# Kernel tuning notes

Measured on AMD Instinct MI355X. Metric: run time of the kernel, lower is better.

Reference implementation:

```python
import jax, jax.numpy as jnp
import numpy as np

N = 100_000      # nodes
E = 1_600_000    # directed input edges (no self loops, unique canonical pairs)
F_IN = 256       # num_features
HID = 128        # 2 * num_hidden (GATConv out width)
NHID = 64        # num_hidden
C = 4            # num_classes
G = 128          # number of graphs in the batch
NEG_SLOPE = 0.2  # PyG GATConv default LeakyReLU slope


def setup_inputs() -> dict:
    key = jax.random.key(0)
    ks = jax.random.split(key, 16)

    # --- graph structure (numpy; deduped canonical pairs so that
    # concat(e, reversed(e)) exactly matches PyG to_undirected+coalesce) ---
    rng = np.random.RandomState(0)
    n_cand = int(E * 1.05)
    s = rng.randint(0, N, size=n_cand)
    off = rng.randint(1, N, size=n_cand)
    d = (s + off) % N                      # guarantees no self loops
    lo, hi = np.minimum(s, d), np.maximum(s, d)
    pairs = np.unique(lo.astype(np.int64) * N + hi.astype(np.int64))[:E]
    src = (pairs // N).astype(np.int64)
    dst = (pairs % N).astype(np.int64)
    edge_index = jnp.asarray(np.stack([src, dst]))  # [2, E]

    batch = jnp.sort(jax.random.randint(ks[0], (N,), 0, G)).astype(jnp.int64)
    x = jax.random.normal(ks[1], (N, F_IN), dtype=jnp.float32)

    sc = 0.05
    params = dict(
        W1=jax.random.normal(ks[2], (HID, F_IN)) * sc,
        as1=jax.random.normal(ks[3], (HID,)) * sc,
        ad1=jax.random.normal(ks[4], (HID,)) * sc,
        b1=jnp.zeros((HID,), jnp.float32),
        W2=jax.random.normal(ks[5], (HID, HID)) * sc,
        as2=jax.random.normal(ks[6], (HID,)) * sc,
        ad2=jax.random.normal(ks[7], (HID,)) * sc,
        b2=jnp.zeros((HID,), jnp.float32),
        fw1=jax.random.normal(ks[8], (NHID, HID)) * sc,
        fb1=jnp.zeros((NHID,), jnp.float32),
        fw2=jax.random.normal(ks[9], (C, NHID)) * sc,
        fb2=jnp.zeros((C,), jnp.float32),
    )
    return dict(x=x, edge_index=edge_index, batch=batch, **params)


def _gat_conv(h_in, src, dst, W, a_src, a_dst, bias):
    """PyG GATConv, heads=1, concat=True. src/dst include self loops."""
    h = h_in @ W.T                                        # [N, out]
    # per-edge attention logits: a_src . h_j + a_dst . h_i
    e = jax.nn.leaky_relu((h @ a_src)[src] + (h @ a_dst)[dst], NEG_SLOPE)
    # edge softmax over incoming edges of each dst node
    m = jax.ops.segment_max(e, dst, num_segments=N)       # [N]
    w = jnp.exp(e - m[dst])
    denom = jax.ops.segment_sum(w, dst, num_segments=N)   # [N] (>0: self loops)
    alpha = w / denom[dst]                                # [Etot]
    out = jax.ops.segment_sum(h[src] * alpha[:, None], dst, num_segments=N)
    return out + bias


def reference(x, edge_index, batch,
              W1, as1, ad1, b1, W2, as2, ad2, b2,
              fw1, fb1, fw2, fb2):
    # to_undirected: input has unique canonical (lo<hi) pairs -> concat exact
    s0, d0 = edge_index[0], edge_index[1]
    loop = jnp.arange(N, dtype=s0.dtype)
    src = jnp.concatenate([s0, d0, loop])  # GATConv adds self loops
    dst = jnp.concatenate([d0, s0, loop])

    h = jax.nn.selu(_gat_conv(x, src, dst, W1, as1, ad1, b1))
    h = jax.nn.selu(_gat_conv(h, src, dst, W2, as2, ad2, b2))

    # global mean pool over graphs
    sums = jax.ops.segment_sum(h, batch, num_segments=G)            # [G, HID]
    cnt = jax.ops.segment_sum(jnp.ones((N,), h.dtype), batch, num_segments=G)
    g = jax.nn.selu(sums / jnp.maximum(cnt, 1.0)[:, None])

    g = jax.nn.selu(g @ fw1.T + fb1)
    # dropout p=0.5 is identity in eval mode
    logits = g @ fw2.T + fb2
    return jax.nn.log_softmax(logits, axis=-1)                      # [G, C]
```

## Files before the change

### kernel.cpp

```cpp
#include <hip/hip_runtime.h>
#include <hip/hip_bf16.h>


#define NN 100000
#define EE 1600000
#define GG 128
#define HID 128
#define AGG_CAP 512
#define NEG_SLOPE 0.2f

__device__ __forceinline__ float lrelu(float x) { return x > 0.f ? x : NEG_SLOPE * x; }

__device__ __forceinline__ float selu(float x) {
    const float sc = 1.0507009873554805f, al = 1.6732632423543772f;
    return x > 0.f ? sc * x : sc * al * (__expf(x) - 1.f);
}

__device__ __forceinline__ unsigned short f2bf(float x) {
    unsigned int b = __float_as_uint(x);
    b += 0x7FFFu + ((b >> 16) & 1u);
    return (unsigned short)(b >> 16);
}


__global__ __launch_bounds__(256) void loptr_kernel(const int* __restrict__ ei,
                                                    int* __restrict__ loptr, int n, int E_) {
    int v = blockIdx.x * blockDim.x + threadIdx.x;
    if (v > n) return;
    int lo = 0, hi = E_;
    while (lo < hi) {
        int mid = (lo + hi) >> 1;
        if (ei[mid] < v) lo = mid + 1; else hi = mid;
    }
    loptr[v] = lo;
}


__global__ void count_kernel(const int* __restrict__ ei, int* __restrict__ deg, int E_) {
    int e = blockIdx.x * blockDim.x + threadIdx.x;
    if (e >= E_) return;
    atomicAdd(&deg[ei[E_ + e]], 1);
}

#define SCAN_CHUNK 512

__global__ __launch_bounds__(256) void block_sum_kernel(const int* __restrict__ deg,
                                                        int* __restrict__ bsum, int n) {
    __shared__ int sd[256];
    int b = blockIdx.x, t = threadIdx.x;
    int base = b * SCAN_CHUNK;
    int v = 0;
    int i0 = base + t, i1 = base + t + 256;
    if (i0 < n) v += deg[i0];
    if (i1 < n) v += deg[i1];
    sd[t] = v;
    __syncthreads();
    for (int off = 128; off; off >>= 1) {
        if (t < off) sd[t] += sd[t + off];
        __syncthreads();
    }
    if (t == 0) bsum[b] = sd[0];
}

__global__ __launch_bounds__(256) void top_scan_kernel(const int* __restrict__ bsum,
                                                       int* __restrict__ boff, int nb,
                                                       int* __restrict__ total_out) {
    __shared__ int a[256], b[256];
    int t = threadIdx.x;
    int v = (t < nb) ? bsum[t] : 0;
    int* cur = a; int* nxt = b;
    cur[t] = v;
    __syncthreads();
    for (int off = 1; off < 256; off <<= 1) {
        int val = cur[t] + ((t >= off) ? cur[t - off] : 0);
        nxt[t] = val;
        __syncthreads();
        int* tmp = cur; cur = nxt; nxt = tmp;
    }
    if (t < nb) boff[t] = cur[t] - v;
    if (t == nb - 1) *total_out = cur[t];
}

__global__ __launch_bounds__(512) void scan_final_kernel(const int* __restrict__ deg,
                                                         const int* __restrict__ boff,
                                                         int* __restrict__ row_ptr,
                                                         int* __restrict__ cursor, int n) {
    __shared__ int a[512], b[512];
    int blk = blockIdx.x, t = threadIdx.x;
    int i = blk * 512 + t;
    int v = (i < n) ? deg[i] : 0;
    int orig = v;
    int* cur = a; int* nxt = b;
    cur[t] = v;
    __syncthreads();
    for (int off = 1; off < 512; off <<= 1) {
        int val = cur[t] + ((t >= off) ? cur[t - off] : 0);
        nxt[t] = val;
        __syncthreads();
        int* tmp = cur; cur = nxt; nxt = tmp;
    }
    if (i < n) {
        int excl = cur[t] - orig + boff[blk];
        row_ptr[i] = excl;
        cursor[i] = excl;
    }
}

__global__ void scatter_kernel(const int* __restrict__ ei, int* __restrict__ cursor,
                               int* __restrict__ csr, int E_) {
    int e = blockIdx.x * blockDim.x + threadIdx.x;
    if (e >= E_) return;
    int u = ei[e], v = ei[E_ + e];
    int p = atomicAdd(&cursor[v], 1);
    csr[p] = u;
}


__global__ __launch_bounds__(256) void sgemm_nt(const float* __restrict__ A,
                                                const float* __restrict__ W,
                                                float* __restrict__ C,
                                                unsigned short* __restrict__ Cb,
                                                int M, int K) {
    __shared__ float As[32][128];
    __shared__ float Bs[32][128];
    int tid = threadIdx.x;
    int brow = blockIdx.x * 128;
    int tx = tid & 15, ty = tid >> 4;
    int lrow = tid >> 3;
    int lk4 = (tid & 7) << 2;
    float acc[8][8];
    #pragma unroll
    for (int i = 0; i < 8; ++i)
        #pragma unroll
        for (int j = 0; j < 8; ++j) acc[i][j] = 0.f;

    int kTiles = K >> 5;
    for (int kt = 0; kt < kTiles; ++kt) {
        int k0 = kt << 5;
        #pragma unroll
        for (int r = 0; r < 4; ++r) {
            int row = lrow + r * 32;
            int grow = brow + row;
            float4 v = make_float4(0.f, 0.f, 0.f, 0.f);
            if (grow < M) v = *reinterpret_cast<const float4*>(A + (size_t)grow * K + k0 + lk4);
            As[lk4 + 0][row] = v.x; As[lk4 + 1][row] = v.y;
            As[lk4 + 2][row] = v.z; As[lk4 + 3][row] = v.w;
        }
        #pragma unroll
        for (int r = 0; r < 4; ++r) {
            int col = lrow + r * 32;
            float4 v = *reinterpret_cast<const float4*>(W + (size_t)col * K + k0 + lk4);
            Bs[lk4 + 0][col] = v.x; Bs[lk4 + 1][col] = v.y;
            Bs[lk4 + 2][col] = v.z; Bs[lk4 + 3][col] = v.w;
        }
        __syncthreads();
        #pragma unroll
        for (int kk = 0; kk < 32; ++kk) {
            float ra[8], rb[8];
            #pragma unroll
            for (int i = 0; i < 8; ++i) ra[i] = As[kk][ty * 8 + i];
            #pragma unroll
            for (int j = 0; j < 8; ++j) rb[j] = Bs[kk][tx * 8 + j];
            #pragma unroll
            for (int i = 0; i < 8; ++i)
                #pragma unroll
                for (int j = 0; j < 8; ++j)
                    acc[i][j] = fmaf(ra[i], rb[j], acc[i][j]);
        }
        __syncthreads();
    }
    #pragma unroll
    for (int i = 0; i < 8; ++i) {
        int grow = brow + ty * 8 + i;
        if (grow < M) {
            float4* o = reinterpret_cast<float4*>(C + (size_t)grow * 128 + tx * 8);
            o[0] = make_float4(acc[i][0], acc[i][1], acc[i][2], acc[i][3]);
            o[1] = make_float4(acc[i][4], acc[i][5], acc[i][6], acc[i][7]);
            union { unsigned short u[8]; float4 f; } pk;
            #pragma unroll
            for (int j = 0; j < 8; ++j) pk.u[j] = f2bf(acc[i][j]);
            *reinterpret_cast<float4*>(Cb + (size_t)grow * 128 + tx * 8) = pk.f;
        }
    }
}


__global__ __launch_bounds__(256) void hshd_kernel(const float* __restrict__ h,
                                                   const float* __restrict__ a_src,
                                                   const float* __restrict__ a_dst,
                                                   float* __restrict__ hs, float* __restrict__ hd,
                                                   int n) {
    int w = (blockIdx.x * blockDim.x + threadIdx.x) >> 6;
    int lane = threadIdx.x & 63;
    if (w >= n) return;
    float2 hv = reinterpret_cast<const float2*>(h + (size_t)w * 128)[lane];
    float2 as2 = reinterpret_cast<const float2*>(a_src)[lane];
    float2 ad2 = reinterpret_cast<const float2*>(a_dst)[lane];
    float ps = hv.x * as2.x + hv.y * as2.y;
    float pd = hv.x * ad2.x + hv.y * ad2.y;
    #pragma unroll
    for (int off = 32; off; off >>= 1) {
        ps += __shfl_xor(ps, off);
        pd += __shfl_xor(pd, off);
    }
    if (lane == 0) { hs[w] = ps; hd[w] = pd; }
}


__global__ __launch_bounds__(256) void agg_kernel(const float* __restrict__ h,
                                                  const unsigned int* __restrict__ hb32,
                                                  const float* __restrict__ hs,
                                                  const float* __restrict__ hd,
                                                  const int* __restrict__ loptr,
                                                  const int* __restrict__ eiD,
                                                  const int* __restrict__ hiptr,
                                                  const int* __restrict__ csr,
                                                  const float* __restrict__ bias,
                                                  float* __restrict__ out, int n) {
    __shared__ float esh[4][AGG_CAP];
    __shared__ int ush[4][AGG_CAP];
    int wib = threadIdx.x >> 6;
    int lane = threadIdx.x & 63;
    int v = blockIdx.x * 4 + wib;
    if (v >= n) return;
    int s_lo = loptr[v];
    int dlo = loptr[v + 1] - s_lo;
    int s_hi = hiptr[v];
    int d = dlo + (hiptr[v + 1] - s_hi);
    float hdv = hd[v];
    float e_self = lrelu(hs[v] + hdv);
    float m, inv;
    bool fits = (d <= AGG_CAP);

    auto nbr = [&](int k) -> int {
        return (k < dlo) ? eiD[s_lo + k] : csr[s_hi + k - dlo];
    };
    auto gx = [&](int u) -> float2 {
        unsigned int w = hb32[(size_t)u * 64 + lane];
        return make_float2(__uint_as_float(w << 16), __uint_as_float(w & 0xFFFF0000u));
    };

    if (fits) {
        float mloc = -3.4e38f;
        for (int k = lane; k < d; k += 64) {
            int u = nbr(k);
            float e = lrelu(hs[u] + hdv);
            ush[wib][k] = u;
            esh[wib][k] = e;
            mloc = fmaxf(mloc, e);
        }
        #pragma unroll
        for (int off = 32; off; off >>= 1) mloc = fmaxf(mloc, __shfl_xor(mloc, off));
        m = fmaxf(mloc, e_self);
        float sloc = 0.f;
        for (int k = lane; k < d; k += 64) sloc += __expf(esh[wib][k] - m);
        #pragma unroll
        for (int off = 32; off; off >>= 1) sloc += __shfl_xor(sloc, off);
        float s = sloc + __expf(e_self - m);
        inv = 1.f / s;
        for (int k = lane; k < d; k += 64) esh[wib][k] = __expf(esh[wib][k] - m) * inv;
    } else {
        float mloc = -3.4e38f;
        for (int k = lane; k < d; k += 64) mloc = fmaxf(mloc, lrelu(hs[nbr(k)] + hdv));
        #pragma unroll
        for (int off = 32; off; off >>= 1) mloc = fmaxf(mloc, __shfl_xor(mloc, off));
        m = fmaxf(mloc, e_self);
        float sloc = 0.f;
        for (int k = lane; k < d; k += 64) sloc += __expf(lrelu(hs[nbr(k)] + hdv) - m);
        #pragma unroll
        for (int off = 32; off; off >>= 1) sloc += __shfl_xor(sloc, off);
        float s = sloc + __expf(e_self - m);
        inv = 1.f / s;
    }
    __syncthreads();

    float2 hvv = reinterpret_cast<const float2*>(h + (size_t)v * 128)[lane];
    float a_self = __expf(e_self - m) * inv;
    float accx = a_self * hvv.x;
    float accy = a_self * hvv.y;
    if (fits) {
        int k = 0;
        for (; k + 4 <= d; k += 4) {
            float a0 = esh[wib][k + 0], a1 = esh[wib][k + 1];
            float a2 = esh[wib][k + 2], a3 = esh[wib][k + 3];
            int u0 = ush[wib][k + 0], u1 = ush[wib][k + 1];
            int u2 = ush[wib][k + 2], u3 = ush[wib][k + 3];
            float2 x0 = gx(u0);
            float2 x1 = gx(u1);
            float2 x2 = gx(u2);
            float2 x3 = gx(u3);
            accx = fmaf(a0, x0.x, accx); accy = fmaf(a0, x0.y, accy);
            accx = fmaf(a1, x1.x, accx); accy = fmaf(a1, x1.y, accy);
            accx = fmaf(a2, x2.x, accx); accy = fmaf(a2, x2.y, accy);
            accx = fmaf(a3, x3.x, accx); accy = fmaf(a3, x3.y, accy);
        }
        for (; k < d; ++k) {
            float al = esh[wib][k];
            float2 xv = gx(ush[wib][k]);
            accx = fmaf(al, xv.x, accx);
            accy = fmaf(al, xv.y, accy);
        }
    } else {
        for (int k = 0; k < d; ++k) {
            int u = nbr(k);
            float al = __expf(lrelu(hs[u] + hdv) - m) * inv;
            float2 xv = gx(u);
            accx = fmaf(al, xv.x, accx);
            accy = fmaf(al, xv.y, accy);
        }
    }
    float2 bb = reinterpret_cast<const float2*>(bias)[lane];
    float o0 = selu(accx + bb.x);
    float o1 = selu(accy + bb.y);
    reinterpret_cast<float2*>(out + (size_t)v * 128)[lane] = make_float2(o0, o1);
}


__device__ __forceinline__ int lower_bound_dev(const int* __restrict__ b, int n, int val) {
    int lo = 0, hi = n;
    while (lo < hi) {
        int mid = (lo + hi) >> 1;
        if (b[mid] < val) lo = mid + 1; else hi = mid;
    }
    return lo;
}

__global__ __launch_bounds__(1024) void pool_mlp_kernel(const float* __restrict__ h,
                                                        const int* __restrict__ batch,
                                                        const float* __restrict__ fw1,
                                                        const float* __restrict__ fb1,
                                                        const float* __restrict__ fw2,
                                                        const float* __restrict__ fb2,
                                                        float* __restrict__ out, int n) {
    int g = blockIdx.x;
    int t = threadIdx.x;
    int lane = t & 63;
    int rg = t >> 6;
    __shared__ float2 sm[16][64];
    __shared__ float gv[128];
    __shared__ float hid[64];
    __shared__ float logits[4];

    int s = lower_bound_dev(batch, n, g);
    int e = lower_bound_dev(batch, n, g + 1);

    float2 acc = make_float2(0.f, 0.f);
    const float2* h2 = reinterpret_cast<const float2*>(h);
    int i = s + rg;
    for (; i + 16 < e; i += 32) {
        float2 v0 = h2[(size_t)i * 64 + lane];
        float2 v1 = h2[(size_t)(i + 16) * 64 + lane];
        acc.x += v0.x + v1.x;
        acc.y += v0.y + v1.y;
    }
    for (; i < e; i += 16) {
        float2 v0 = h2[(size_t)i * 64 + lane];
        acc.x += v0.x;
        acc.y += v0.y;
    }
    sm[rg][lane] = acc;
    __syncthreads();
    if (rg == 0) {
        float2 tot = make_float2(0.f, 0.f);
        #pragma unroll
        for (int r = 0; r < 16; ++r) {
            tot.x += sm[r][lane].x;
            tot.y += sm[r][lane].y;
        }
        float cnt = fmaxf((float)(e - s), 1.0f);
        gv[lane * 2 + 0] = selu(tot.x / cnt);
        gv[lane * 2 + 1] = selu(tot.y / cnt);
    }
    __syncthreads();
    if (t < 64) {
        float a = fb1[t];
        for (int k = 0; k < 128; ++k) a = fmaf(fw1[t * 128 + k], gv[k], a);
        hid[t] = selu(a);
    }
    __syncthreads();
    if (t < 4) {
        float a = fb2[t];
        for (int k = 0; k < 64; ++k) a = fmaf(fw2[t * 64 + k], hid[k], a);
        logits[t] = a;
    }
    __syncthreads();
    if (t < 4) {
        float mx = fmaxf(fmaxf(logits[0], logits[1]), fmaxf(logits[2], logits[3]));
        float sum = __expf(logits[0] - mx) + __expf(logits[1] - mx) +
                    __expf(logits[2] - mx) + __expf(logits[3] - mx);
        out[g * 4 + t] = logits[t] - mx - logf(sum);
    }
}


extern "C" void kernel_launch(void* const* d_in, const int* in_sizes, int n_in,
                              void* d_out, int out_size, void* d_ws, size_t ws_size,
                              hipStream_t stream) {
    const float* x   = (const float*)d_in[0];
    const int*   ei  = (const int*)d_in[1];
    const int*   bat = (const int*)d_in[2];
    const float* W1  = (const float*)d_in[3];
    const float* as1 = (const float*)d_in[4];
    const float* ad1 = (const float*)d_in[5];
    const float* b1  = (const float*)d_in[6];
    const float* W2  = (const float*)d_in[7];
    const float* as2 = (const float*)d_in[8];
    const float* ad2 = (const float*)d_in[9];
    const float* b2  = (const float*)d_in[10];
    const float* fw1 = (const float*)d_in[11];
    const float* fb1 = (const float*)d_in[12];
    const float* fw2 = (const float*)d_in[13];
    const float* fb2 = (const float*)d_in[14];
    float* out = (float*)d_out;

    char* ws = (char*)d_ws;
    size_t off = 0;
    auto alloc = [&](size_t bytes) {
        void* p = ws + off;
        off += (bytes + 255) & ~(size_t)255;
        return p;
    };
    float*          bufA    = (float*)alloc((size_t)NN * 128 * 4);
    float*          bufB    = (float*)alloc((size_t)NN * 128 * 4);
    unsigned short* hb      = (unsigned short*)alloc((size_t)NN * 128 * 2);
    float*          hs      = (float*)alloc((size_t)NN * 4);
    float*          hd      = (float*)alloc((size_t)NN * 4);
    int*            deg     = (int*)alloc((size_t)NN * 4);
    int*            row_ptr = (int*)alloc((size_t)(NN + 1) * 4);
    int*            cursor  = (int*)alloc((size_t)NN * 4);
    int*            loptr   = (int*)alloc((size_t)(NN + 1) * 4);
    int*            csr     = (int*)alloc((size_t)EE * 4);
    int*            bsum    = (int*)alloc(256 * 4);
    int*            boff    = (int*)alloc(256 * 4);

    hipMemsetAsync(deg, 0, (size_t)NN * 4, stream);
    loptr_kernel<<<(NN + 1 + 255) / 256, 256, 0, stream>>>(ei, loptr, NN, EE);
    count_kernel<<<(EE + 255) / 256, 256, 0, stream>>>(ei, deg, EE);
    int NB = (NN + SCAN_CHUNK - 1) / SCAN_CHUNK;
    block_sum_kernel<<<NB, 256, 0, stream>>>(deg, bsum, NN);
    top_scan_kernel<<<1, 256, 0, stream>>>(bsum, boff, NB, row_ptr + NN);
    scan_final_kernel<<<NB, 512, 0, stream>>>(deg, boff, row_ptr, cursor, NN);
    scatter_kernel<<<(EE + 255) / 256, 256, 0, stream>>>(ei, cursor, csr, EE);

    const int* eiD = ei + EE;

    sgemm_nt<<<(NN + 127) / 128, 256, 0, stream>>>(x, W1, bufA, hb, NN, 256);
    hshd_kernel<<<((size_t)NN * 64 + 255) / 256, 256, 0, stream>>>(bufA, as1, ad1, hs, hd, NN);
    agg_kernel<<<(NN + 3) / 4, 256, 0, stream>>>(bufA, (const unsigned int*)hb, hs, hd,
                                                 loptr, eiD, row_ptr, csr, b1, bufB, NN);

    sgemm_nt<<<(NN + 127) / 128, 256, 0, stream>>>(bufB, W2, bufA, hb, NN, 128);
    hshd_kernel<<<((size_t)NN * 64 + 255) / 256, 256, 0, stream>>>(bufA, as2, ad2, hs, hd, NN);
    agg_kernel<<<(NN + 3) / 4, 256, 0, stream>>>(bufA, (const unsigned int*)hb, hs, hd,
                                                 loptr, eiD, row_ptr, csr, b2, bufB, NN);

    pool_mlp_kernel<<<GG, 1024, 0, stream>>>(bufB, bat, fw1, fb1, fw2, fb2, out, NN);
}
```

Baseline: 828.8 us.

## Replace FP32 SIMT GEMMs with bf16 MFMA GEMMs and bf16 layer-2 input

```diff
diff --git a/kernel.cpp b/kernel.cpp
--- a/kernel.cpp
+++ b/kernel.cpp
@@ -9,6 +9,9 @@
 #define AGG_CAP 512
 #define NEG_SLOPE 0.2f
 
+typedef short bf16x8 __attribute__((ext_vector_type(8)));
+typedef float f32x4 __attribute__((ext_vector_type(4)));
+
 __device__ __forceinline__ float lrelu(float x) { return x > 0.f ? x : NEG_SLOPE * x; }
 
 __device__ __forceinline__ float selu(float x) {
@@ -20,6 +23,17 @@
     unsigned int b = __float_as_uint(x);
     b += 0x7FFFu + ((b >> 16) & 1u);
     return (unsigned short)(b >> 16);
+}
+
+
+__global__ __launch_bounds__(256) void castbf_kernel(const float* __restrict__ in,
+                                                     unsigned short* __restrict__ out, int n) {
+    int i = (blockIdx.x * blockDim.x + threadIdx.x) * 4;
+    if (i >= n) return;
+    float4 v = *reinterpret_cast<const float4*>(in + i);
+    union { unsigned short u[4]; uint2 w; } pk;
+    pk.u[0] = f2bf(v.x); pk.u[1] = f2bf(v.y); pk.u[2] = f2bf(v.z); pk.u[3] = f2bf(v.w);
+    *reinterpret_cast<uint2*>(out + i) = pk.w;
 }
 
 
@@ -116,70 +130,98 @@
 }
 
 
-__global__ __launch_bounds__(256) void sgemm_nt(const float* __restrict__ A,
-                                                const float* __restrict__ W,
-                                                float* __restrict__ C,
-                                                unsigned short* __restrict__ Cb,
-                                                int M, int K) {
-    __shared__ float As[32][128];
-    __shared__ float Bs[32][128];
+template<int K, bool BF16IN>
+__global__ __launch_bounds__(256) void mfma_gemm(const void* __restrict__ Ain,
+                                                 const unsigned short* __restrict__ Wb,
+                                                 float* __restrict__ C,
+                                                 unsigned short* __restrict__ Cb,
+                                                 int M) {
+    __shared__ unsigned short As[128 * 32];
+    __shared__ unsigned short Bs[128 * 32];
     int tid = threadIdx.x;
     int brow = blockIdx.x * 128;
-    int tx = tid & 15, ty = tid >> 4;
-    int lrow = tid >> 3;
-    int lk4 = (tid & 7) << 2;
-    float acc[8][8];
+    int w = tid >> 6, lane = tid & 63;
+    int wr = (w >> 1) * 64, wc = (w & 1) * 64;
+    int l15 = lane & 15, g = lane >> 4;
+
+    const f32x4 zero = {0.f, 0.f, 0.f, 0.f};
+    f32x4 acc[4][4];
     #pragma unroll
-    for (int i = 0; i < 8; ++i)
-        #pragma unroll
-        for (int j = 0; j < 8; ++j) acc[i][j] = 0.f;
-
-    int kTiles = K >> 5;
-    for (int kt = 0; kt < kTiles; ++kt) {
-        int k0 = kt << 5;
-        #pragma unroll
-        for (int r = 0; r < 4; ++r) {
-            int row = lrow + r * 32;
-            int grow = brow + row;
-            float4 v = make_float4(0.f, 0.f, 0.f, 0.f);
-            if (grow < M) v = *reinterpret_cast<const float4*>(A + (size_t)grow * K + k0 + lk4);
-            As[lk4 + 0][row] = v.x; As[lk4 + 1][row] = v.y;
-            As[lk4 + 2][row] = v.z; As[lk4 + 3][row] = v.w;
-        }
-        #pragma unroll
-        for (int r = 0; r < 4; ++r) {
-            int col = lrow + r * 32;
-            float4 v = *reinterpret_cast<const float4*>(W + (size_t)col * K + k0 + lk4);
-            Bs[lk4 + 0][col] = v.x; Bs[lk4 + 1][col] = v.y;
-            Bs[lk4 + 2][col] = v.z; Bs[lk4 + 3][col] = v.w;
+    for (int m = 0; m < 4; ++m)
+        #pragma unroll
+        for (int n = 0; n < 4; ++n) acc[m][n] = zero;
+
+    int srow = tid >> 2;
+    int slot = tid & 3;
+
+    for (int k0 = 0; k0 < K; k0 += 32) {
+        #pragma unroll
+        for (int half = 0; half < 2; ++half) {
+            int r = srow + half * 64;
+            int grow = brow + r;
+            union { unsigned short u[8]; uint4 v; } pk;
+            if (BF16IN) {
+                const unsigned short* A16 = (const unsigned short*)Ain;
+                if (grow < M)
+                    pk.v = *reinterpret_cast<const uint4*>(A16 + (size_t)grow * K + k0 + slot * 8);
+                else pk.v = make_uint4(0, 0, 0, 0);
+            } else {
+                const float* A32 = (const float*)Ain;
+                if (grow < M) {
+                    const float4* p = reinterpret_cast<const float4*>(A32 + (size_t)grow * K + k0 + slot * 8);
+                    float4 f0 = p[0], f1 = p[1];
+                    pk.u[0] = f2bf(f0.x); pk.u[1] = f2bf(f0.y);
+                    pk.u[2] = f2bf(f0.z); pk.u[3] = f2bf(f0.w);
+                    pk.u[4] = f2bf(f1.x); pk.u[5] = f2bf(f1.y);
+                    pk.u[6] = f2bf(f1.z); pk.u[7] = f2bf(f1.w);
+                } else pk.v = make_uint4(0, 0, 0, 0);
+            }
+            int ss = slot ^ (r & 3);
+            *reinterpret_cast<uint4*>(&As[r * 32 + ss * 8]) = pk.v;
+        }
+        #pragma unroll
+        for (int half = 0; half < 2; ++half) {
+            int r = srow + half * 64;
+            uint4 v = *reinterpret_cast<const uint4*>(Wb + (size_t)r * K + k0 + slot * 8);
+            int ss = slot ^ (r & 3);
+            *reinterpret_cast<uint4*>(&Bs[r * 32 + ss * 8]) = v;
         }
         __syncthreads();
-        #pragma unroll
-        for (int kk = 0; kk < 32; ++kk) {
-            float ra[8], rb[8];
+
+        bf16x8 af[4], bfr[4];
+        #pragma unroll
+        for (int m = 0; m < 4; ++m) {
+            int row = wr + m * 16 + l15;
+            af[m] = *reinterpret_cast<const bf16x8*>(&As[row * 32 + ((g ^ (row & 3)) * 8)]);
+        }
+        #pragma unroll
+        for (int n = 0; n < 4; ++n) {
+            int col = wc + n * 16 + l15;
+            bfr[n] = *reinterpret_cast<const bf16x8*>(&Bs[col * 32 + ((g ^ (col & 3)) * 8)]);
+        }
+        #pragma unroll
+        for (int m = 0; m < 4; ++m)
             #pragma unroll
-            for (int i = 0; i < 8; ++i) ra[i] = As[kk][ty * 8 + i];
-            #pragma unroll
-            for (int j = 0; j < 8; ++j) rb[j] = Bs[kk][tx * 8 + j];
-            #pragma unroll
-            for (int i = 0; i < 8; ++i)
+            for (int n = 0; n < 4; ++n)
+                acc[m][n] = __builtin_amdgcn_mfma_f32_16x16x32_bf16(af[m], bfr[n], acc[m][n], 0, 0, 0);
+        __syncthreads();
+    }
+
+    #pragma unroll
+    for (int m = 0; m < 4; ++m) {
+        int rbase = brow + wr + m * 16 + g * 4;
+        #pragma unroll
+        for (int j = 0; j < 4; ++j) {
+            int row = rbase + j;
+            if (row < M) {
                 #pragma unroll
-                for (int j = 0; j < 8; ++j)
-                    acc[i][j] = fmaf(ra[i], rb[j], acc[i][j]);
-        }
-        __syncthreads();
-    }
-    #pragma unroll
-    for (int i = 0; i < 8; ++i) {
-        int grow = brow + ty * 8 + i;
-        if (grow < M) {
-            float4* o = reinterpret_cast<float4*>(C + (size_t)grow * 128 + tx * 8);
-            o[0] = make_float4(acc[i][0], acc[i][1], acc[i][2], acc[i][3]);
-            o[1] = make_float4(acc[i][4], acc[i][5], acc[i][6], acc[i][7]);
-            union { unsigned short u[8]; float4 f; } pk;
-            #pragma unroll
-            for (int j = 0; j < 8; ++j) pk.u[j] = f2bf(acc[i][j]);
-            *reinterpret_cast<float4*>(Cb + (size_t)grow * 128 + tx * 8) = pk.f;
+                for (int n = 0; n < 4; ++n) {
+                    int col = wc + n * 16 + l15;
+                    float val = acc[m][n][j];
+                    C[(size_t)row * 128 + col] = val;
+                    Cb[(size_t)row * 128 + col] = f2bf(val);
+                }
+            }
         }
     }
 }
@@ -216,7 +258,9 @@
                                                   const int* __restrict__ hiptr,
                                                   const int* __restrict__ csr,
                                                   const float* __restrict__ bias,
-                                                  float* __restrict__ out, int n) {
+                                                  float* __restrict__ out,
+                                                  unsigned int* __restrict__ outb,
+                                                  int n) {
     __shared__ float esh[4][AGG_CAP];
     __shared__ int ush[4][AGG_CAP];
     int wib = threadIdx.x >> 6;
@@ -313,6 +357,8 @@
     float o0 = selu(accx + bb.x);
     float o1 = selu(accy + bb.y);
     reinterpret_cast<float2*>(out + (size_t)v * 128)[lane] = make_float2(o0, o1);
+    unsigned int pb = ((unsigned int)f2bf(o1) << 16) | (unsigned int)f2bf(o0);
+    outb[(size_t)v * 64 + lane] = pb;
 }
 
 
@@ -423,6 +469,9 @@
     float*          bufA    = (float*)alloc((size_t)NN * 128 * 4);
     float*          bufB    = (float*)alloc((size_t)NN * 128 * 4);
     unsigned short* hb      = (unsigned short*)alloc((size_t)NN * 128 * 2);
+    unsigned short* hbB     = (unsigned short*)alloc((size_t)NN * 128 * 2);
+    unsigned short* wb1     = (unsigned short*)alloc((size_t)HID * 256 * 2);
+    unsigned short* wb2     = (unsigned short*)alloc((size_t)HID * 128 * 2);
     float*          hs      = (float*)alloc((size_t)NN * 4);
     float*          hd      = (float*)alloc((size_t)NN * 4);
     int*            deg     = (int*)alloc((size_t)NN * 4);
@@ -442,17 +491,23 @@
     scan_final_kernel<<<NB, 512, 0, stream>>>(deg, boff, row_ptr, cursor, NN);
     scatter_kernel<<<(EE + 255) / 256, 256, 0, stream>>>(ei, cursor, csr, EE);
 
+    castbf_kernel<<<(HID * 256 / 4 + 255) / 256, 256, 0, stream>>>(W1, wb1, HID * 256);
+    castbf_kernel<<<(HID * 128 / 4 + 255) / 256, 256, 0, stream>>>(W2, wb2, HID * 128);
+
     const int* eiD = ei + EE;
-
-    sgemm_nt<<<(NN + 127) / 128, 256, 0, stream>>>(x, W1, bufA, hb, NN, 256);
+    int gemmGrid = (NN + 127) / 128;
+
+    mfma_gemm<256, false><<<gemmGrid, 256, 0, stream>>>(x, wb1, bufA, hb, NN);
     hshd_kernel<<<((size_t)NN * 64 + 255) / 256, 256, 0, stream>>>(bufA, as1, ad1, hs, hd, NN);
     agg_kernel<<<(NN + 3) / 4, 256, 0, stream>>>(bufA, (const unsigned int*)hb, hs, hd,
-                                                 loptr, eiD, row_ptr, csr, b1, bufB, NN);
-
-    sgemm_nt<<<(NN + 127) / 128, 256, 0, stream>>>(bufB, W2, bufA, hb, NN, 128);
+                                                 loptr, eiD, row_ptr, csr, b1, bufB,
+                                                 (unsigned int*)hbB, NN);
+
+    mfma_gemm<128, true><<<gemmGrid, 256, 0, stream>>>(hbB, wb2, bufA, hb, NN);
     hshd_kernel<<<((size_t)NN * 64 + 255) / 256, 256, 0, stream>>>(bufA, as2, ad2, hs, hd, NN);
     agg_kernel<<<(NN + 3) / 4, 256, 0, stream>>>(bufA, (const unsigned int*)hb, hs, hd,
-                                                 loptr, eiD, row_ptr, csr, b2, bufB, NN);
+                                                 loptr, eiD, row_ptr, csr, b2, bufB,
+                                                 (unsigned int*)hbB, NN);
 
     pool_mlp_kernel<<<GG, 1024, 0, stream>>>(bufB, bat, fw1, fb1, fw2, fb2, out, NN);
 }
```

Result: faster. 739.8 us (-10.7%).
